# Kernel tuning notes

Hardware: AMD Instinct MI355X
Metric: run time of the kernel (lower is better)

Reference implementation:

```python
import jax, jax.numpy as jnp
import numpy as np

N_WIN = 232
T = 8
KERNEL = (2, 2, 2)
STRIDE = (2, 2, 2)
SLOPE = 25.0  # fast_sigmoid surrogate slope


@jax.custom_vjp
def spike(v):
    # heaviside(v) with fast-sigmoid surrogate gradient
    return (v > 0).astype(v.dtype)

def _spike_fwd(v):
    return spike(v), v

def _spike_bwd(v, g):
    return (g / (SLOPE * jnp.abs(v) + 1.0) ** 2,)

spike.defvjp(_spike_fwd, _spike_bwd)


def _avg_pool3d(x, kernel, stride):
    # x: (B, C, D, H, W), VALID pooling
    win = (1, 1) + tuple(kernel)
    st = (1, 1) + tuple(stride)
    s = jax.lax.reduce_window(x, 0.0, jax.lax.add, win, st, 'VALID')
    return s / float(np.prod(kernel))


def setup_inputs() -> dict:
    key = jax.random.key(0)
    ks = jax.random.split(key, 14)
    B, C, H, W = 64, 3, 32, 32
    input_dim, h0, h1, n_cls = 256, 256, 128, 6
    x = jax.random.normal(ks[0], (B, C, N_WIN, H, W), jnp.float32)
    W_in = jax.random.normal(ks[1], (h0, input_dim), jnp.float32) * 0.05
    b_in = jnp.zeros((h0,), jnp.float32)
    W_hid = jax.random.normal(ks[2], (h1, h0), jnp.float32) * 0.05
    b_hid = jnp.zeros((h1,), jnp.float32)
    in_feat = C * h1 * 14  # C * hidden[1] * D'
    W_out = jax.random.normal(ks[3], (n_cls, in_feat), jnp.float32) * 0.05
    b_out = jnp.zeros((n_cls,), jnp.float32)
    beta_in = jax.random.uniform(ks[4], (h0,), jnp.float32)
    thr_in = jax.random.uniform(ks[5], (h0,), jnp.float32)
    beta_hid = jax.random.uniform(ks[6], (h1,), jnp.float32)
    thr_hid = jax.random.uniform(ks[7], (h1,), jnp.float32)
    beta_out = jax.random.uniform(ks[8], (n_cls,), jnp.float32)
    return dict(x=x, W_in=W_in, b_in=b_in, W_hid=W_hid, b_hid=b_hid,
                W_out=W_out, b_out=b_out, beta_in=beta_in, thr_in=thr_in,
                beta_hid=beta_hid, thr_hid=thr_hid, beta_out=beta_out)


def _lif(mem, cur, beta, thr):
    # snntorch Leaky, reset-by-subtract; reset uses detached prev-mem spike
    reset = jax.lax.stop_gradient((mem > thr).astype(mem.dtype))
    mem = jnp.clip(beta, 0.0, 1.0) * mem + cur - reset * thr
    spk = spike(mem - thr)
    return spk, mem


def reference(x, W_in, b_in, W_hid, b_hid, W_out, b_out,
              beta_in, thr_in, beta_hid, thr_hid, beta_out):
    B, C, _, H, W = x.shape
    chunk = N_WIN // T  # 29
    # split depth into T chunks: (T, B, C, chunk, H, W)
    xt = x.reshape(B, C, T, chunk, H, W).transpose(2, 0, 1, 3, 4, 5)
    pooled = jax.vmap(lambda v: _avg_pool3d(v, KERNEL, STRIDE))(xt)  # (T,B,C,D',H',W')
    _, _, _, Dp, Hp, Wp = pooled.shape
    pr = pooled.reshape(T, B, C * Dp, Hp * Wp)
    # fc_in applied to all timesteps at once (recurrence-free)
    cur_in_all = jnp.einsum('tbnf,hf->tbnh', pr, W_in) + b_in  # (T,B,N,h0)

    h0 = W_in.shape[0]
    h1 = W_hid.shape[0]
    n_cls = W_out.shape[0]
    N = C * Dp
    mem_in0 = jnp.zeros((B, N, h0), x.dtype)
    mem_hid0 = jnp.zeros((B, N, h1), x.dtype)
    mem_out0 = jnp.zeros((B, n_cls), x.dtype)

    def step(carry, cur_in):
        mem_in, mem_hid, mem_out = carry
        spk_in, mem_in = _lif(mem_in, cur_in, beta_in, thr_in)
        cur_hid = jnp.einsum('bnh,gh->bng', spk_in, W_hid) + b_hid
        spk_hid, mem_hid = _lif(mem_hid, cur_hid, beta_hid, thr_hid)
        flat = spk_hid.reshape(spk_hid.shape[0], -1)  # (B, N*h1)
        cur_out = flat @ W_out.T + b_out
        spk_out, mem_out = _lif(mem_out, cur_out, beta_out, jnp.float32(1.0))
        return (mem_in, mem_hid, mem_out), spk_out

    _, spk_rec = jax.lax.scan(step, (mem_in0, mem_hid0, mem_out0), cur_in_all)
    return spk_rec  # (T, B, n_classes)
```

## Files before the change

### kernel.cpp

```cpp
#include <hip/hip_runtime.h>

#define T_STEPS 8
#define NROW    42
#define BN      2688
#define H0      256
#define H1      128
#define KFLAT   5376


#define SWA(r)  ((r) + ((r) >> 5) * 4)

__global__ __launch_bounds__(512, 4) void pool_gemm_lif(
        const float* __restrict__ x,
        const float* __restrict__ B,
        const float* __restrict__ bias,
        const float* __restrict__ beta,
        const float* __restrict__ thr,
        float* __restrict__ spk) {
    __shared__ float At[16 * 68];
    __shared__ float Bt[16 * 284];
    int tid = threadIdx.x;
    int gbase = blockIdx.x * 8;

    int wp = tid & 15;
    int q  = tid >> 4;
    const float* xb0;
    const float* xb1;
    int mloc0 = q * 2, mloc1 = q * 2 + 1;
    {
        int g = gbase + (mloc0 >> 3);
        int t = mloc0 & 7;
        int b = g / 42, r = g - b * 42;
        int c = r / 14, dp = r - c * 14;
        xb0 = x + ((long)b * 712704 + (long)c * 237568
                + (long)(t * 29 + 2 * dp) * 1024 + 2 * wp);
    }
    {
        int g = gbase + (mloc1 >> 3);
        int t = mloc1 & 7;
        int b = g / 42, r = g - b * 42;
        int c = r / 14, dp = r - c * 14;
        xb1 = x + ((long)b * 712704 + (long)c * 237568
                + (long)(t * 29 + 2 * dp) * 1024 + 2 * wp);
    }
    int acol0 = SWA(mloc0), acol1 = SWA(mloc1);

    int bn0 = tid >> 1;
    int bq  = tid & 1;
    const float* Bp = B + (long)bn0 * 256 + bq * 8;
    int bcol = SWA(bn0);

    int tm = tid & 7, tn = tid >> 3;
    int ca = SWA(tm * 8);
    int cb = SWA(tn * 4);

    float acc[8][4] = {};

    for (int k0 = 0; k0 < 256; k0 += 16) {
        int hp = k0 >> 4;
        const float* p0 = xb0 + hp * 64;
        const float* p1 = xb1 + hp * 64;
        float2 a00 = *(const float2*)(p0);
        float2 a01 = *(const float2*)(p0 + 32);
        float2 a02 = *(const float2*)(p0 + 1024);
        float2 a03 = *(const float2*)(p0 + 1056);
        float2 a10 = *(const float2*)(p1);
        float2 a11 = *(const float2*)(p1 + 32);
        float2 a12 = *(const float2*)(p1 + 1024);
        float2 a13 = *(const float2*)(p1 + 1056);
        float4 w0 = *(const float4*)(Bp + k0);
        float4 w1 = *(const float4*)(Bp + k0 + 4);
        __syncthreads();
        float s0 = a00.x + a00.y + a01.x + a01.y + a02.x + a02.y + a03.x + a03.y;
        float s1 = a10.x + a10.y + a11.x + a11.y + a12.x + a12.y + a13.x + a13.y;
        At[wp * 68 + acol0] = s0 * 0.125f;
        At[wp * 68 + acol1] = s1 * 0.125f;
        int kb = bq * 8;
        Bt[(kb + 0) * 284 + bcol] = w0.x; Bt[(kb + 1) * 284 + bcol] = w0.y;
        Bt[(kb + 2) * 284 + bcol] = w0.z; Bt[(kb + 3) * 284 + bcol] = w0.w;
        Bt[(kb + 4) * 284 + bcol] = w1.x; Bt[(kb + 5) * 284 + bcol] = w1.y;
        Bt[(kb + 6) * 284 + bcol] = w1.z; Bt[(kb + 7) * 284 + bcol] = w1.w;
        __syncthreads();
#pragma unroll
        for (int k = 0; k < 16; ++k) {
            float4 av0 = *(const float4*)&At[k * 68 + ca];
            float4 av1 = *(const float4*)&At[k * 68 + ca + 4];
            float4 bv  = *(const float4*)&Bt[k * 284 + cb];
            float am[8] = {av0.x, av0.y, av0.z, av0.w, av1.x, av1.y, av1.z, av1.w};
            float bb[4] = {bv.x, bv.y, bv.z, bv.w};
#pragma unroll
            for (int i = 0; i < 8; ++i)
#pragma unroll
                for (int j = 0; j < 4; ++j)
                    acc[i][j] = fmaf(am[i], bb[j], acc[i][j]);
        }
    }

#pragma unroll
    for (int j = 0; j < 4; ++j) {
        int h = tn * 4 + j;
        float be = fminf(fmaxf(beta[h], 0.f), 1.f);
        float th = thr[h];
        float bi = bias[h];
        float mem = 0.f;
#pragma unroll
        for (int t = 0; t < T_STEPS; ++t) {
            float cur = acc[t][j] + bi;
            float reset = (mem > th) ? th : 0.f;
            mem = be * mem + cur - reset;
            acc[t][j] = ((mem - th) > 0.f) ? 1.f : 0.f;
        }
    }
    int rbase = blockIdx.x * 64 + tm * 8;
#pragma unroll
    for (int t = 0; t < T_STEPS; ++t) {
        float4 o = {acc[t][0], acc[t][1], acc[t][2], acc[t][3]};
        *(float4*)&spk[(long)(rbase + t) * 256 + tn * 4] = o;
    }
}

__global__ __launch_bounds__(256, 4) void gemm_lif64(
        const float* __restrict__ A,
        const float* __restrict__ B,
        const float* __restrict__ bias,
        const float* __restrict__ beta,
        const float* __restrict__ thr,
        float* __restrict__ spk) {
    __shared__ float At[16 * 68];
    __shared__ float Bt[16 * 140];
    int tid = threadIdx.x;
    int m0 = blockIdx.x * 64;

    int sr = tid >> 2, sq = tid & 3;
    const float* Ap = A + (long)(m0 + sr) * 256 + sq * 4;
    int acolS = SWA(sr);

    int br = tid >> 1, bq = tid & 1;
    const float* Bp = B + (long)br * 256 + bq * 8;
    int bcolS = SWA(br);

    int tm = tid & 7, tn = tid >> 3;
    int ca = SWA(tm * 8);
    int cb = SWA(tn * 4);

    float acc[8][4] = {};

    for (int k0 = 0; k0 < 256; k0 += 16) {
        float4 a  = *(const float4*)(Ap + k0);
        float4 w0 = *(const float4*)(Bp + k0);
        float4 w1 = *(const float4*)(Bp + k0 + 4);
        __syncthreads();
        int ka = sq * 4;
        At[(ka + 0) * 68 + acolS] = a.x; At[(ka + 1) * 68 + acolS] = a.y;
        At[(ka + 2) * 68 + acolS] = a.z; At[(ka + 3) * 68 + acolS] = a.w;
        int kb = bq * 8;
        Bt[(kb + 0) * 140 + bcolS] = w0.x; Bt[(kb + 1) * 140 + bcolS] = w0.y;
        Bt[(kb + 2) * 140 + bcolS] = w0.z; Bt[(kb + 3) * 140 + bcolS] = w0.w;
        Bt[(kb + 4) * 140 + bcolS] = w1.x; Bt[(kb + 5) * 140 + bcolS] = w1.y;
        Bt[(kb + 6) * 140 + bcolS] = w1.z; Bt[(kb + 7) * 140 + bcolS] = w1.w;
        __syncthreads();
#pragma unroll
        for (int k = 0; k < 16; ++k) {
            float4 av0 = *(const float4*)&At[k * 68 + ca];
            float4 av1 = *(const float4*)&At[k * 68 + ca + 4];
            float4 bv  = *(const float4*)&Bt[k * 140 + cb];
            float am[8] = {av0.x, av0.y, av0.z, av0.w, av1.x, av1.y, av1.z, av1.w};
            float bb[4] = {bv.x, bv.y, bv.z, bv.w};
#pragma unroll
            for (int i = 0; i < 8; ++i)
#pragma unroll
                for (int j = 0; j < 4; ++j)
                    acc[i][j] = fmaf(am[i], bb[j], acc[i][j]);
        }
    }

#pragma unroll
    for (int j = 0; j < 4; ++j) {
        int h = tn * 4 + j;
        float be = fminf(fmaxf(beta[h], 0.f), 1.f);
        float th = thr[h];
        float bi = bias[h];
        float mem = 0.f;
#pragma unroll
        for (int t = 0; t < T_STEPS; ++t) {
            float cur = acc[t][j] + bi;
            float reset = (mem > th) ? th : 0.f;
            mem = be * mem + cur - reset;
            acc[t][j] = ((mem - th) > 0.f) ? 1.f : 0.f;
        }
    }
    int rbase = m0 + tm * 8;
#pragma unroll
    for (int t = 0; t < T_STEPS; ++t) {
        float4 o = {acc[t][0], acc[t][1], acc[t][2], acc[t][3]};
        *(float4*)&spk[(long)(rbase + t) * 128 + tn * 4] = o;
    }
}

__global__ __launch_bounds__(256) void out_gemm(const float* __restrict__ spkh,
                                                const float* __restrict__ W_out,
                                                const float* __restrict__ b_out,
                                                float* __restrict__ cur_out) {
    __shared__ float part[256][8];
    int row = blockIdx.x;
    int t = row >> 6, b = row & 63;
    int tid = threadIdx.x;
    float acc[6] = {0.f, 0.f, 0.f, 0.f, 0.f, 0.f};
    for (int j = tid; j < KFLAT; j += 256) {
        int n = j >> 7, h = j & 127;
        float s = spkh[((long)(b * NROW + n) * 8 + t) * 128 + h];
#pragma unroll
        for (int c = 0; c < 6; ++c)
            acc[c] = fmaf(s, W_out[c * KFLAT + j], acc[c]);
    }
#pragma unroll
    for (int c = 0; c < 6; ++c) part[tid][c] = acc[c];
    __syncthreads();
    for (int off = 128; off > 0; off >>= 1) {
        if (tid < off) {
#pragma unroll
            for (int c = 0; c < 6; ++c) part[tid][c] += part[tid + off][c];
        }
        __syncthreads();
    }
    if (tid < 6) cur_out[row * 6 + tid] = part[0][tid] + b_out[tid];
}

__global__ void lif_out_kernel(const float* __restrict__ cur_out,
                               const float* __restrict__ beta_out,
                               float* __restrict__ out) {
    int j = threadIdx.x;
    if (j >= 384) return;
    int cls = j % 6;
    float be = fminf(fmaxf(beta_out[cls], 0.f), 1.f);
    float mem = 0.f;
#pragma unroll
    for (int t = 0; t < T_STEPS; ++t) {
        float cur = cur_out[t * 384 + j];
        float reset = (mem > 1.f) ? 1.f : 0.f;
        mem = be * mem + cur - reset;
        out[t * 384 + j] = ((mem - 1.f) > 0.f) ? 1.f : 0.f;
    }
}

extern "C" void kernel_launch(void* const* d_in, const int* in_sizes, int n_in,
                              void* d_out, int out_size, void* d_ws, size_t ws_size,
                              hipStream_t stream) {
    (void)in_sizes; (void)n_in; (void)out_size; (void)ws_size;
    const float* x        = (const float*)d_in[0];
    const float* W_in     = (const float*)d_in[1];
    const float* b_in     = (const float*)d_in[2];
    const float* W_hid    = (const float*)d_in[3];
    const float* b_hid    = (const float*)d_in[4];
    const float* W_out    = (const float*)d_in[5];
    const float* b_out    = (const float*)d_in[6];
    const float* beta_in  = (const float*)d_in[7];
    const float* thr_in   = (const float*)d_in[8];
    const float* beta_hid = (const float*)d_in[9];
    const float* thr_hid  = (const float*)d_in[10];
    const float* beta_out = (const float*)d_in[11];
    float* out = (float*)d_out;

    float* buf0 = (float*)d_ws;
    float* buf1 = buf0 + 5505024;
    float* curo = buf1 + 5505024;

    pool_gemm_lif<<<336, 512, 0, stream>>>(x, W_in, b_in, beta_in, thr_in, buf1);
    gemm_lif64<<<336, 256, 0, stream>>>(buf1, W_hid, b_hid, beta_hid, thr_hid, buf0);
    out_gemm<<<512, 256, 0, stream>>>(buf0, W_out, b_out, curo);
    lif_out_kernel<<<1, 384, 0, stream>>>(curo, beta_out, out);
}
```

Baseline: 356.8 us.

## Fuse input-layer and hidden-layer GEMM+LIF into one kernel via shared memory

Merges the pooled fc_in GEMM+LIF and the fc_hid GEMM+LIF into a single kernel. Input-layer spikes stay in shared memory, so the intermediate spike tensor is no longer written to and read back from global memory. The block tile shrinks from 64 to 32 rows with 256 threads, doubling the grid to 672 blocks. This adds more shared memory per block and re-streams W_in and W_hid once per smaller tile, so weight traffic per output row rises.

Result: faster. 342.5 us (-4.0%).

```diff
diff --git a/kernel.cpp b/kernel.cpp
--- a/kernel.cpp
+++ b/kernel.cpp
@@ -10,17 +10,25 @@
 
 #define SWA(r)  ((r) + ((r) >> 5) * 4)
 
-__global__ __launch_bounds__(512, 4) void pool_gemm_lif(
+__global__ __launch_bounds__(256, 3) void snn_front(
         const float* __restrict__ x,
-        const float* __restrict__ B,
-        const float* __restrict__ bias,
-        const float* __restrict__ beta,
-        const float* __restrict__ thr,
-        float* __restrict__ spk) {
-    __shared__ float At[16 * 68];
-    __shared__ float Bt[16 * 284];
+        const float* __restrict__ Wi,
+        const float* __restrict__ bi,
+        const float* __restrict__ beti,
+        const float* __restrict__ thri,
+        const float* __restrict__ Wh,
+        const float* __restrict__ bh,
+        const float* __restrict__ beth,
+        const float* __restrict__ thrh,
+        float* __restrict__ spkh) {
+    __shared__ float smem[9216 + 2240];
+    float* S   = smem;
+    float* At  = smem;
+    float* Bt  = smem + 576;
+    float* Bt2 = smem + 9216;
+
     int tid = threadIdx.x;
-    int gbase = blockIdx.x * 8;
+    int gbase = blockIdx.x * 4;
 
     int wp = tid & 15;
     int q  = tid >> 4;
@@ -43,15 +51,13 @@
         xb1 = x + ((long)b * 712704 + (long)c * 237568
                 + (long)(t * 29 + 2 * dp) * 1024 + 2 * wp);
     }
-    int acol0 = SWA(mloc0), acol1 = SWA(mloc1);
-
-    int bn0 = tid >> 1;
-    int bq  = tid & 1;
-    const float* Bp = B + (long)bn0 * 256 + bq * 8;
-    int bcol = SWA(bn0);
-
-    int tm = tid & 7, tn = tid >> 3;
-    int ca = SWA(tm * 8);
+
+    const float* Bp = Wi + (long)tid * 256;
+    int bcol = SWA(tid);
+
+    int tm = tid & 3;
+    int tn = tid >> 2;
+    int ca = tm * 8;
     int cb = SWA(tn * 4);
 
     float acc[8][4] = {};
@@ -70,21 +76,26 @@
         float2 a13 = *(const float2*)(p1 + 1056);
         float4 w0 = *(const float4*)(Bp + k0);
         float4 w1 = *(const float4*)(Bp + k0 + 4);
+        float4 w2 = *(const float4*)(Bp + k0 + 8);
+        float4 w3 = *(const float4*)(Bp + k0 + 12);
         __syncthreads();
         float s0 = a00.x + a00.y + a01.x + a01.y + a02.x + a02.y + a03.x + a03.y;
         float s1 = a10.x + a10.y + a11.x + a11.y + a12.x + a12.y + a13.x + a13.y;
-        At[wp * 68 + acol0] = s0 * 0.125f;
-        At[wp * 68 + acol1] = s1 * 0.125f;
-        int kb = bq * 8;
-        Bt[(kb + 0) * 284 + bcol] = w0.x; Bt[(kb + 1) * 284 + bcol] = w0.y;
-        Bt[(kb + 2) * 284 + bcol] = w0.z; Bt[(kb + 3) * 284 + bcol] = w0.w;
-        Bt[(kb + 4) * 284 + bcol] = w1.x; Bt[(kb + 5) * 284 + bcol] = w1.y;
-        Bt[(kb + 6) * 284 + bcol] = w1.z; Bt[(kb + 7) * 284 + bcol] = w1.w;
+        At[wp * 36 + mloc0] = s0 * 0.125f;
+        At[wp * 36 + mloc1] = s1 * 0.125f;
+        Bt[ 0 * 284 + bcol] = w0.x; Bt[ 1 * 284 + bcol] = w0.y;
+        Bt[ 2 * 284 + bcol] = w0.z; Bt[ 3 * 284 + bcol] = w0.w;
+        Bt[ 4 * 284 + bcol] = w1.x; Bt[ 5 * 284 + bcol] = w1.y;
+        Bt[ 6 * 284 + bcol] = w1.z; Bt[ 7 * 284 + bcol] = w1.w;
+        Bt[ 8 * 284 + bcol] = w2.x; Bt[ 9 * 284 + bcol] = w2.y;
+        Bt[10 * 284 + bcol] = w2.z; Bt[11 * 284 + bcol] = w2.w;
+        Bt[12 * 284 + bcol] = w3.x; Bt[13 * 284 + bcol] = w3.y;
+        Bt[14 * 284 + bcol] = w3.z; Bt[15 * 284 + bcol] = w3.w;
         __syncthreads();
 #pragma unroll
         for (int k = 0; k < 16; ++k) {
-            float4 av0 = *(const float4*)&At[k * 68 + ca];
-            float4 av1 = *(const float4*)&At[k * 68 + ca + 4];
+            float4 av0 = *(const float4*)&At[k * 36 + ca];
+            float4 av1 = *(const float4*)&At[k * 36 + ca + 4];
             float4 bv  = *(const float4*)&Bt[k * 284 + cb];
             float am[8] = {av0.x, av0.y, av0.z, av0.w, av1.x, av1.y, av1.z, av1.w};
             float bb[4] = {bv.x, bv.y, bv.z, bv.w};
@@ -99,101 +110,77 @@
 #pragma unroll
     for (int j = 0; j < 4; ++j) {
         int h = tn * 4 + j;
-        float be = fminf(fmaxf(beta[h], 0.f), 1.f);
-        float th = thr[h];
-        float bi = bias[h];
+        float be = fminf(fmaxf(beti[h], 0.f), 1.f);
+        float th = thri[h];
+        float bb = bi[h];
         float mem = 0.f;
 #pragma unroll
         for (int t = 0; t < T_STEPS; ++t) {
-            float cur = acc[t][j] + bi;
+            float cur = acc[t][j] + bb;
             float reset = (mem > th) ? th : 0.f;
             mem = be * mem + cur - reset;
             acc[t][j] = ((mem - th) > 0.f) ? 1.f : 0.f;
         }
     }
-    int rbase = blockIdx.x * 64 + tm * 8;
-#pragma unroll
-    for (int t = 0; t < T_STEPS; ++t) {
-        float4 o = {acc[t][0], acc[t][1], acc[t][2], acc[t][3]};
-        *(float4*)&spk[(long)(rbase + t) * 256 + tn * 4] = o;
-    }
-}
-
-__global__ __launch_bounds__(256, 4) void gemm_lif64(
-        const float* __restrict__ A,
-        const float* __restrict__ B,
-        const float* __restrict__ bias,
-        const float* __restrict__ beta,
-        const float* __restrict__ thr,
-        float* __restrict__ spk) {
-    __shared__ float At[16 * 68];
-    __shared__ float Bt[16 * 140];
-    int tid = threadIdx.x;
-    int m0 = blockIdx.x * 64;
-
-    int sr = tid >> 2, sq = tid & 3;
-    const float* Ap = A + (long)(m0 + sr) * 256 + sq * 4;
-    int acolS = SWA(sr);
-
-    int br = tid >> 1, bq = tid & 1;
-    const float* Bp = B + (long)br * 256 + bq * 8;
-    int bcolS = SWA(br);
-
-    int tm = tid & 7, tn = tid >> 3;
-    int ca = SWA(tm * 8);
-    int cb = SWA(tn * 4);
-
-    float acc[8][4] = {};
-
-    for (int k0 = 0; k0 < 256; k0 += 16) {
-        float4 a  = *(const float4*)(Ap + k0);
-        float4 w0 = *(const float4*)(Bp + k0);
-        float4 w1 = *(const float4*)(Bp + k0 + 4);
-        __syncthreads();
-        int ka = sq * 4;
-        At[(ka + 0) * 68 + acolS] = a.x; At[(ka + 1) * 68 + acolS] = a.y;
-        At[(ka + 2) * 68 + acolS] = a.z; At[(ka + 3) * 68 + acolS] = a.w;
-        int kb = bq * 8;
-        Bt[(kb + 0) * 140 + bcolS] = w0.x; Bt[(kb + 1) * 140 + bcolS] = w0.y;
-        Bt[(kb + 2) * 140 + bcolS] = w0.z; Bt[(kb + 3) * 140 + bcolS] = w0.w;
-        Bt[(kb + 4) * 140 + bcolS] = w1.x; Bt[(kb + 5) * 140 + bcolS] = w1.y;
-        Bt[(kb + 6) * 140 + bcolS] = w1.z; Bt[(kb + 7) * 140 + bcolS] = w1.w;
-        __syncthreads();
-#pragma unroll
-        for (int k = 0; k < 16; ++k) {
-            float4 av0 = *(const float4*)&At[k * 68 + ca];
-            float4 av1 = *(const float4*)&At[k * 68 + ca + 4];
-            float4 bv  = *(const float4*)&Bt[k * 140 + cb];
-            float am[8] = {av0.x, av0.y, av0.z, av0.w, av1.x, av1.y, av1.z, av1.w};
-            float bb[4] = {bv.x, bv.y, bv.z, bv.w};
-#pragma unroll
-            for (int i = 0; i < 8; ++i)
-#pragma unroll
-                for (int j = 0; j < 4; ++j)
-                    acc[i][j] = fmaf(am[i], bb[j], acc[i][j]);
-        }
-    }
-
+
+    __syncthreads();
 #pragma unroll
     for (int j = 0; j < 4; ++j) {
         int h = tn * 4 + j;
-        float be = fminf(fmaxf(beta[h], 0.f), 1.f);
-        float th = thr[h];
-        float bi = bias[h];
+#pragma unroll
+        for (int t = 0; t < T_STEPS; ++t)
+            S[h * 36 + ca + t] = acc[t][j];
+    }
+
+    const float* Bp2 = Wh + (long)(tid >> 1) * 256 + (tid & 1) * 8;
+    int bcol2 = SWA(tid >> 1);
+    int cb2 = SWA(tn * 2);
+    float acc2[8][2] = {};
+
+    for (int k0 = 0; k0 < 256; k0 += 16) {
+        float4 u0 = *(const float4*)(Bp2 + k0);
+        float4 u1 = *(const float4*)(Bp2 + k0 + 4);
+        __syncthreads();
+        int kb = (tid & 1) * 8;
+        Bt2[(kb + 0) * 140 + bcol2] = u0.x; Bt2[(kb + 1) * 140 + bcol2] = u0.y;
+        Bt2[(kb + 2) * 140 + bcol2] = u0.z; Bt2[(kb + 3) * 140 + bcol2] = u0.w;
+        Bt2[(kb + 4) * 140 + bcol2] = u1.x; Bt2[(kb + 5) * 140 + bcol2] = u1.y;
+        Bt2[(kb + 6) * 140 + bcol2] = u1.z; Bt2[(kb + 7) * 140 + bcol2] = u1.w;
+        __syncthreads();
+#pragma unroll
+        for (int k = 0; k < 16; ++k) {
+            float4 av0 = *(const float4*)&S[(k0 + k) * 36 + ca];
+            float4 av1 = *(const float4*)&S[(k0 + k) * 36 + ca + 4];
+            float2 bv  = *(const float2*)&Bt2[k * 140 + cb2];
+            float am[8] = {av0.x, av0.y, av0.z, av0.w, av1.x, av1.y, av1.z, av1.w};
+#pragma unroll
+            for (int i = 0; i < 8; ++i) {
+                acc2[i][0] = fmaf(am[i], bv.x, acc2[i][0]);
+                acc2[i][1] = fmaf(am[i], bv.y, acc2[i][1]);
+            }
+        }
+    }
+
+#pragma unroll
+    for (int j = 0; j < 2; ++j) {
+        int h = tn * 2 + j;
+        float be = fminf(fmaxf(beth[h], 0.f), 1.f);
+        float th = thrh[h];
+        float bb = bh[h];
         float mem = 0.f;
 #pragma unroll
         for (int t = 0; t < T_STEPS; ++t) {
-            float cur = acc[t][j] + bi;
+            float cur = acc2[t][j] + bb;
             float reset = (mem > th) ? th : 0.f;
             mem = be * mem + cur - reset;
-            acc[t][j] = ((mem - th) > 0.f) ? 1.f : 0.f;
-        }
-    }
-    int rbase = m0 + tm * 8;
+            acc2[t][j] = ((mem - th) > 0.f) ? 1.f : 0.f;
+        }
+    }
+    int rbase = blockIdx.x * 32 + tm * 8;
 #pragma unroll
     for (int t = 0; t < T_STEPS; ++t) {
-        float4 o = {acc[t][0], acc[t][1], acc[t][2], acc[t][3]};
-        *(float4*)&spk[(long)(rbase + t) * 128 + tn * 4] = o;
+        float2 o = {acc2[t][0], acc2[t][1]};
+        *(float2*)&spkh[(long)(rbase + t) * 128 + tn * 2] = o;
     }
 }
 
@@ -262,11 +249,10 @@
     float* out = (float*)d_out;
 
     float* buf0 = (float*)d_ws;
-    float* buf1 = buf0 + 5505024;
-    float* curo = buf1 + 5505024;
-
-    pool_gemm_lif<<<336, 512, 0, stream>>>(x, W_in, b_in, beta_in, thr_in, buf1);
-    gemm_lif64<<<336, 256, 0, stream>>>(buf1, W_hid, b_hid, beta_hid, thr_hid, buf0);
+    float* curo = buf0 + 2752512;
+
+    snn_front<<<672, 256, 0, stream>>>(x, W_in, b_in, beta_in, thr_in,
+                                       W_hid, b_hid, beta_hid, thr_hid, buf0);
     out_gemm<<<512, 256, 0, stream>>>(buf0, W_out, b_out, curo);
     lif_out_kernel<<<1, 384, 0, stream>>>(curo, beta_out, out);
 }
```
